# Kernel tuning notes

Measured on AMD Instinct MI355X. Metric: run time of the kernel, lower is better.

Reference implementation:

```python
import jax, jax.numpy as jnp
import numpy as np


def setup_inputs() -> dict:
    key = jax.random.key(0)
    kq, kk, kv, km = jax.random.split(key, 4)
    B, H, S, D = 2, 16, 2048, 64
    q = jax.random.normal(kq, (B, H, S, D), dtype=jnp.float32)
    k = jax.random.normal(kk, (B, H, S, D), dtype=jnp.float32)
    v = jax.random.normal(kv, (B, H, S, D), dtype=jnp.float32)
    mask = jax.random.randint(km, (B, 1, S, D * S // D), 0, 2).astype(bool)
    return {"q": q, "k": k, "v": v, "mask": mask, "d_k": 64}


def reference(q, k, v, mask, d_k):
    # score = q @ k^T / sqrt(d_k), masked_fill(mask, -1e9)
    scale = jnp.float32(1.0 / np.sqrt(d_k))
    score = jnp.einsum("bhsd,bhtd->bhst", q, k) * scale  # [B,H,S,S]
    score = jnp.where(mask, jnp.float32(-1e9), score)
    attention = jax.nn.softmax(score, axis=-1)
    # NOTE: original module (faithfully) multiplies the RAW masked score by v,
    # not the softmaxed attention: results = score @ v
    results = jnp.einsum("bhst,bhtd->bhsd", score, v)
    return (results, attention)
```

## Files before the change

kernel.cpp:

```cpp
#include <hip/hip_runtime.h>

typedef __attribute__((ext_vector_type(8))) short short8;
typedef __attribute__((ext_vector_type(4))) float f32x4;

#define S_LEN 2048
#define DH 64

__device__ __forceinline__ unsigned short f2bf(float x) {
  unsigned u = __builtin_bit_cast(unsigned, x);
  u += 0x7fffu + ((u >> 16) & 1u);
  return (unsigned short)(u >> 16);
}

__global__ void detect_stride_k(const unsigned char* __restrict__ m, int* flag) {
  __shared__ int any;
  if (threadIdx.x == 0) any = 0;
  __syncthreads();
  int acc = 0;
  for (int i = threadIdx.x; i < 4096; i += 256)
    if (i & 3) acc |= m[i];
  if (acc) atomicOr(&any, 1);
  __syncthreads();
  if (threadIdx.x == 0) *flag = any ? 1 : 4;
}

__global__ void prep_kernel(const float* __restrict__ k,
                            const float* __restrict__ v,
                            const unsigned char* __restrict__ m,
                            const int* __restrict__ flagp,
                            char* __restrict__ kbf,
                            char* __restrict__ vtbf,
                            unsigned* __restrict__ bits) {
  int bid = blockIdx.x;
  if (bid < 2048) {
    int idx = bid * 256 + threadIdx.x;
    const float4* s = (const float4*)k + (size_t)idx * 2;
    float4 a = s[0], b = s[1];
    int4 o;
    o.x = (int)f2bf(a.x) | ((int)f2bf(a.y) << 16);
    o.y = (int)f2bf(a.z) | ((int)f2bf(a.w) << 16);
    o.z = (int)f2bf(b.x) | ((int)f2bf(b.y) << 16);
    o.w = (int)f2bf(b.z) | ((int)f2bf(b.w) << 16);
    ((int4*)kbf)[idx] = o;
  } else if (bid < 6144) {
    int gt = (bid - 2048) * 256 + threadIdx.x;
    int wid = gt >> 6;
    int lane = gt & 63;
    int bh = wid >> 9;
    int rem = wid & 511;
    int d0 = (rem >> 5) * 4;
    int t = (rem & 31) * 64 + lane;
    float4 val = *(const float4*)(v + ((size_t)bh * S_LEN + t) * DH + d0);
    unsigned short* o = (unsigned short*)vtbf;
    size_t base = ((size_t)bh * DH + d0) * S_LEN + t;
    o[base]             = f2bf(val.x);
    o[base + S_LEN]     = f2bf(val.y);
    o[base + 2 * S_LEN] = f2bf(val.z);
    o[base + 3 * S_LEN] = f2bf(val.w);
  } else {
    int idx = (bid - 6144) * 256 + threadIdx.x;
    unsigned wword = 0;
    if (*flagp == 1) {
      const uint4* p = (const uint4*)(m + (size_t)idx * 32);
      uint4 a = p[0], bq = p[1];
      unsigned arr[8] = {a.x, a.y, a.z, a.w, bq.x, bq.y, bq.z, bq.w};
#pragma unroll
      for (int d = 0; d < 8; ++d)
#pragma unroll
        for (int j = 0; j < 4; ++j)
          wword |= (((arr[d] >> (8 * j)) & 255u) != 0u ? 1u : 0u) << (d * 4 + j);
    } else {
      const uint4* p = (const uint4*)m + (size_t)idx * 8;
#pragma unroll
      for (int d = 0; d < 8; ++d) {
        uint4 vv = p[d];
        wword |= (vv.x ? 1u : 0u) << (d * 4);
        wword |= (vv.y ? 1u : 0u) << (d * 4 + 1);
        wword |= (vv.z ? 1u : 0u) << (d * 4 + 2);
        wword |= (vv.w ? 1u : 0u) << (d * 4 + 3);
      }
    }
    bits[idx] = wword;
  }
}

__global__ __launch_bounds__(512, 4)
void attn_fused(const float* __restrict__ qsrc,
                const unsigned* __restrict__ mbits,
                const char* __restrict__ kbf,
                const char* __restrict__ vtbf,
                float* __restrict__ out) {
  __shared__ __align__(16) char smem[81920];

  const int tid = threadIdx.x;
  const int lane = tid & 63;
  const int w = tid >> 6;
  const int l15 = lane & 15;
  const int g = lane >> 4;
  const int sw = (l15 & 7) << 4;

  int raw = blockIdx.x;
  int swz = (raw & 7) * 64 + (raw >> 3);
  const int bh = swz >> 4;
  const int qblk = swz & 15;
  const int b = bh >> 4;
  const int q0 = qblk * 128 + w * 16;

  const char* ksrc_bh = kbf + (size_t)bh * (S_LEN * DH * 2);
  const char* vsrc_bh = vtbf + (size_t)bh * (DH * S_LEN * 2);
  char* pb = smem + 65536 + w * 2048;

  const unsigned* mrow = mbits + (size_t)b * (S_LEN * (S_LEN / 32)) +
                         (size_t)(q0 + l15) * (S_LEN / 32);

  auto stageK = [&](int buf, int t0) {
    char* dst = smem + buf * 16384;
#pragma unroll
    for (int it = 0; it < 2; ++it) {
      int o = (w * 2 + it) * 1024 + lane * 16;
      int r = o >> 7;
      int inner = o & 127;
      const char* gp = ksrc_bh + (size_t)t0 * 128 + r * 128 + (inner ^ ((r & 7) << 4));
      __builtin_amdgcn_global_load_lds((const unsigned*)gp,
                                       (unsigned*)(dst + (w * 2 + it) * 1024), 16, 0, 0);
    }
  };
  auto stageV = [&](int buf, int t0) {
    char* dst = smem + 32768 + buf * 16384;
#pragma unroll
    for (int it = 0; it < 2; ++it) {
      int o = (w * 2 + it) * 1024 + lane * 16;
      int r = o >> 8;
      int inner = o & 255;
      const char* gp = vsrc_bh + (size_t)t0 * 2 + (size_t)r * (S_LEN * 2) +
                       (inner ^ ((r & 7) << 4));
      __builtin_amdgcn_global_load_lds((const unsigned*)gp,
                                       (unsigned*)(dst + (w * 2 + it) * 1024), 16, 0, 0);
    }
  };

  short8 qf[2];
#pragma unroll
  for (int kc = 0; kc < 2; ++kc) {
    const float* qp = qsrc + ((size_t)bh * S_LEN + q0 + l15) * DH + 32 * kc + 8 * g;
    float4 x = *(const float4*)qp;
    float4 y = *(const float4*)(qp + 4);
    short8 f;
    f[0] = (short)f2bf(x.x); f[1] = (short)f2bf(x.y);
    f[2] = (short)f2bf(x.z); f[3] = (short)f2bf(x.w);
    f[4] = (short)f2bf(y.x); f[5] = (short)f2bf(y.y);
    f[6] = (short)f2bf(y.z); f[7] = (short)f2bf(y.w);
    qf[kc] = f;
  }

  f32x4 acc[4];
#pragma unroll
  for (int i = 0; i < 4; ++i) acc[i] = (f32x4){0.f, 0.f, 0.f, 0.f};
  float lp = 0.f;

  stageK(0, 0);
  stageV(0, 0);
  uint4 mw = *(const uint4*)mrow;
  __syncthreads();
  int cur = 0;

  for (int t0 = 0; t0 < S_LEN; t0 += 128) {
    uint4 mw_n;
    if (t0 + 128 < S_LEN) {
      stageK(cur ^ 1, t0 + 128);
      stageV(cur ^ 1, t0 + 128);
      mw_n = *(const uint4*)(mrow + (t0 + 128) / 32);
    }
    const char* kbuf = smem + cur * 16384;
    const char* vbuf = smem + 32768 + cur * 16384;

    f32x4 sf[8];
#pragma unroll
    for (int tc = 0; tc < 8; ++tc) {
      const char* rowp = kbuf + (16 * tc + l15) * 128;
      short8 a0 = *(const short8*)(rowp + ((16 * g) ^ sw));
      short8 a1 = *(const short8*)(rowp + ((64 + 16 * g) ^ sw));
      f32x4 z = (f32x4){0.f, 0.f, 0.f, 0.f};
      f32x4 t00 = __builtin_amdgcn_mfma_f32_16x16x32_bf16(a0, qf[0], z, 0, 0, 0);
      sf[tc] = __builtin_amdgcn_mfma_f32_16x16x32_bf16(a1, qf[1], t00, 0, 0, 0);
    }

    const unsigned mwa[4] = {mw.x, mw.y, mw.z, mw.w};
#pragma unroll
    for (int h = 0; h < 2; ++h) {
      char* pbr = pb + l15 * 128;
#pragma unroll
      for (int tq = 0; tq < 4; ++tq) {
        const int tc = 4 * h + tq;
        unsigned nib = (mwa[tc >> 1] >> (16 * (tc & 1) + 4 * g)) & 15u;
        float s0 = (nib & 1u) ? -1e9f : sf[tc][0] * 0.125f;
        float s1 = (nib & 2u) ? -1e9f : sf[tc][1] * 0.125f;
        float s2 = (nib & 4u) ? -1e9f : sf[tc][2] * 0.125f;
        float s3 = (nib & 8u) ? -1e9f : sf[tc][3] * 0.125f;
        lp += __expf(s0) + __expf(s1) + __expf(s2) + __expf(s3);
        int2 pk;
        pk.x = (int)f2bf(s0) | ((int)f2bf(s1) << 16);
        pk.y = (int)f2bf(s2) | ((int)f2bf(s3) << 16);
        *(int2*)(pbr + ((32 * tq + 8 * g) ^ sw)) = pk;
      }
      short8 p0 = *(const short8*)(pb + l15 * 128 + ((16 * g) ^ sw));
      short8 p1 = *(const short8*)(pb + l15 * 128 + ((64 + 16 * g) ^ sw));
#pragma unroll
      for (int dr = 0; dr < 4; ++dr) {
        const char* vr = vbuf + (16 * dr + l15) * 256;
        short8 v0 = *(const short8*)(vr + ((h * 128 + 16 * g) ^ sw));
        short8 v1 = *(const short8*)(vr + ((h * 128 + 64 + 16 * g) ^ sw));
        acc[dr] = __builtin_amdgcn_mfma_f32_16x16x32_bf16(v0, p0, acc[dr], 0, 0, 0);
        acc[dr] = __builtin_amdgcn_mfma_f32_16x16x32_bf16(v1, p1, acc[dr], 0, 0, 0);
      }
    }

    mw = mw_n;
    __syncthreads();
    cur ^= 1;
  }

  float l = lp;
  l += __shfl_xor(l, 16);
  l += __shfl_xor(l, 32);
  const float inv = 1.0f / l;

#pragma unroll
  for (int dr = 0; dr < 4; ++dr) {
    float4 o;
    o.x = acc[dr][0]; o.y = acc[dr][1];
    o.z = acc[dr][2]; o.w = acc[dr][3];
    *(float4*)(out + ((size_t)bh * S_LEN + q0 + l15) * DH + 16 * dr + 4 * g) = o;
  }

  float* att = out + (size_t)4194304 + (size_t)bh * S_LEN * S_LEN;
  stageK(0, 0);
  mw = *(const uint4*)mrow;
  __syncthreads();
  cur = 0;

  const int q = q0 + l15;
  for (int t0 = 0; t0 < S_LEN; t0 += 128) {
    uint4 mw_n;
    if (t0 + 128 < S_LEN) {
      stageK(cur ^ 1, t0 + 128);
      mw_n = *(const uint4*)(mrow + (t0 + 128) / 32);
    }
    const char* kbuf = smem + cur * 16384;
    const unsigned mwa[4] = {mw.x, mw.y, mw.z, mw.w};

#pragma unroll
    for (int tc = 0; tc < 8; ++tc) {
      const char* rowp = kbuf + (16 * tc + l15) * 128;
      short8 a0 = *(const short8*)(rowp + ((16 * g) ^ sw));
      short8 a1 = *(const short8*)(rowp + ((64 + 16 * g) ^ sw));
      f32x4 z = (f32x4){0.f, 0.f, 0.f, 0.f};
      f32x4 t0f = __builtin_amdgcn_mfma_f32_16x16x32_bf16(a0, qf[0], z, 0, 0, 0);
      f32x4 sff = __builtin_amdgcn_mfma_f32_16x16x32_bf16(a1, qf[1], t0f, 0, 0, 0);
      const int t = t0 + 16 * tc + 4 * g;
      unsigned nib = (mwa[tc >> 1] >> (16 * (tc & 1) + 4 * g)) & 15u;
      float s0 = (nib & 1u) ? -1e9f : sff[0] * 0.125f;
      float s1 = (nib & 2u) ? -1e9f : sff[1] * 0.125f;
      float s2 = (nib & 4u) ? -1e9f : sff[2] * 0.125f;
      float s3 = (nib & 8u) ? -1e9f : sff[3] * 0.125f;
      float4 e;
      e.x = __expf(s0) * inv;
      e.y = __expf(s1) * inv;
      e.z = __expf(s2) * inv;
      e.w = __expf(s3) * inv;
      *(float4*)(att + (size_t)q * S_LEN + t) = e;
    }

    mw = mw_n;
    asm volatile("s_waitcnt vmcnt(8)" ::: "memory");
    __builtin_amdgcn_s_barrier();
    __builtin_amdgcn_sched_barrier(0);
    cur ^= 1;
  }
}

extern "C" void kernel_launch(void* const* d_in, const int* in_sizes, int n_in,
                              void* d_out, int out_size, void* d_ws, size_t ws_size,
                              hipStream_t stream) {
  (void)in_sizes; (void)n_in; (void)out_size; (void)ws_size;
  const float* q = (const float*)d_in[0];
  const float* k = (const float*)d_in[1];
  const float* v = (const float*)d_in[2];
  const unsigned char* mask = (const unsigned char*)d_in[3];
  float* out = (float*)d_out;

  char* ws = (char*)d_ws;
  int* flag = (int*)ws;
  char* kbf = ws + 256;
  char* vtbf = ws + 256 + 8 * 1024 * 1024;
  unsigned* bits = (unsigned*)(ws + 256 + 16 * 1024 * 1024);

  detect_stride_k<<<1, 256, 0, stream>>>(mask, flag);
  prep_kernel<<<7168, 256, 0, stream>>>(k, v, mask, flag, kbf, vtbf, bits);
  attn_fused<<<512, 512, 0, stream>>>(q, bits, kbf, vtbf, out);
}
```

Measured before the change: 218.6 us.

## Transpose attention MFMA so stores coalesce along key dimension

Swaps the MFMA operand order in the attention-writing pass so each lane holds four query rows at one key column. Stores become scalar writes that coalesce across 16 lanes along the key dimension, where before each lane wrote a float4 to a different query row. The per-row inverse sums are fetched with shuffles, and mask words are loaded per row inside the loop rather than prefetched. The software-pipelined waitcnt/barrier is replaced by a plain __syncthreads, which may reduce overlap of the K staging.

```diff
diff --git a/kernel.cpp b/kernel.cpp
--- a/kernel.cpp
+++ b/kernel.cpp
@@ -234,47 +234,47 @@
   }
 
   float* att = out + (size_t)4194304 + (size_t)bh * S_LEN * S_LEN;
+
+  float invr[4];
+#pragma unroll
+  for (int r = 0; r < 4; ++r) invr[r] = __shfl(inv, 4 * g + r, 64);
+
+  const unsigned* mrowB = mbits + (size_t)b * (S_LEN * (S_LEN / 32)) +
+                          (size_t)(q0 + 4 * g) * (S_LEN / 32);
+
   stageK(0, 0);
-  mw = *(const uint4*)mrow;
   __syncthreads();
   cur = 0;
 
-  const int q = q0 + l15;
   for (int t0 = 0; t0 < S_LEN; t0 += 128) {
-    uint4 mw_n;
-    if (t0 + 128 < S_LEN) {
-      stageK(cur ^ 1, t0 + 128);
-      mw_n = *(const uint4*)(mrow + (t0 + 128) / 32);
-    }
+    if (t0 + 128 < S_LEN) stageK(cur ^ 1, t0 + 128);
     const char* kbuf = smem + cur * 16384;
-    const unsigned mwa[4] = {mw.x, mw.y, mw.z, mw.w};
+
+    uint4 mv[4];
+#pragma unroll
+    for (int r = 0; r < 4; ++r) mv[r] = *(const uint4*)(mrowB + r * 64 + t0 / 32);
+
+    float* attT = att + (size_t)(q0 + 4 * g) * S_LEN + t0 + l15;
 
 #pragma unroll
     for (int tc = 0; tc < 8; ++tc) {
       const char* rowp = kbuf + (16 * tc + l15) * 128;
-      short8 a0 = *(const short8*)(rowp + ((16 * g) ^ sw));
-      short8 a1 = *(const short8*)(rowp + ((64 + 16 * g) ^ sw));
+      short8 b0 = *(const short8*)(rowp + ((16 * g) ^ sw));
+      short8 b1 = *(const short8*)(rowp + ((64 + 16 * g) ^ sw));
       f32x4 z = (f32x4){0.f, 0.f, 0.f, 0.f};
-      f32x4 t0f = __builtin_amdgcn_mfma_f32_16x16x32_bf16(a0, qf[0], z, 0, 0, 0);
-      f32x4 sff = __builtin_amdgcn_mfma_f32_16x16x32_bf16(a1, qf[1], t0f, 0, 0, 0);
-      const int t = t0 + 16 * tc + 4 * g;
-      unsigned nib = (mwa[tc >> 1] >> (16 * (tc & 1) + 4 * g)) & 15u;
-      float s0 = (nib & 1u) ? -1e9f : sff[0] * 0.125f;
-      float s1 = (nib & 2u) ? -1e9f : sff[1] * 0.125f;
-      float s2 = (nib & 4u) ? -1e9f : sff[2] * 0.125f;
-      float s3 = (nib & 8u) ? -1e9f : sff[3] * 0.125f;
-      float4 e;
-      e.x = __expf(s0) * inv;
-      e.y = __expf(s1) * inv;
-      e.z = __expf(s2) * inv;
-      e.w = __expf(s3) * inv;
-      *(float4*)(att + (size_t)q * S_LEN + t) = e;
-    }
-
-    mw = mw_n;
-    asm volatile("s_waitcnt vmcnt(8)" ::: "memory");
-    __builtin_amdgcn_s_barrier();
-    __builtin_amdgcn_sched_barrier(0);
+      f32x4 t0f = __builtin_amdgcn_mfma_f32_16x16x32_bf16(qf[0], b0, z, 0, 0, 0);
+      f32x4 sff = __builtin_amdgcn_mfma_f32_16x16x32_bf16(qf[1], b1, t0f, 0, 0, 0);
+      const int bitsh = 16 * (tc & 1) + l15;
+#pragma unroll
+      for (int r = 0; r < 4; ++r) {
+        unsigned word = (tc >> 1) == 0 ? mv[r].x : (tc >> 1) == 1 ? mv[r].y
+                      : (tc >> 1) == 2 ? mv[r].z : mv[r].w;
+        float s = ((word >> bitsh) & 1u) ? -1e9f : sff[r] * 0.125f;
+        attT[(size_t)r * S_LEN + 16 * tc] = __expf(s) * invr[r];
+      }
+    }
+
+    __syncthreads();
     cur ^= 1;
   }
 }
```

Measured after the change: 206.7 us. -5.5%, faster.
